# Kernel tuning notes

Hardware: AMD Instinct MI355X
Metric: run time of the kernel (lower is better)

## Reference

```python
import jax, jax.numpy as jnp
import numpy as np

B, S, H, E, K = 4, 4096, 1024, 8, 2


def setup_inputs() -> dict:
    key = jax.random.key(0)
    ks = jax.random.split(key, 5)
    scale = 1.0 / np.sqrt(H)
    return {
        "x": jax.random.normal(ks[0], (B, S, H), dtype=jnp.float32),
        "gate_w": jax.random.normal(ks[1], (H, E), dtype=jnp.float32) * scale,
        "gate_b": jnp.zeros((E,), dtype=jnp.float32),
        "expert_w": jax.random.normal(ks[2], (E, H, H), dtype=jnp.float32) * scale,
        "expert_b": jnp.zeros((E, H), dtype=jnp.float32),
    }


def reference(x, gate_w, gate_b, expert_w, expert_b):
    bsz, seq_len, hsz = x.shape
    h = x.reshape(-1, hsz)                              # [T, H], T = B*S

    # --- router ---
    router_logits = h @ gate_w + gate_b                 # [T, E]
    probs = jax.nn.softmax(router_logits, axis=-1)
    top_w, top_idx = jax.lax.top_k(probs, K)            # [T, K]
    top_w = top_w / jnp.sum(top_w, axis=-1, keepdims=True)

    # combine weight per (token, expert): sum over top-k slots of w * onehot(idx)
    one_hot = jax.nn.one_hot(top_idx, E, dtype=h.dtype)  # [T, K, E]
    combine = jnp.einsum("tk,tke->te", top_w, one_hot)   # [T, E]

    # --- experts (dense grouped GEMM, masked-combined; same math as gather/scatter loop) ---
    expert_out = jnp.einsum("th,ehd->etd", h, expert_w) + expert_b[:, None, :]  # [E, T, H]
    out = jnp.einsum("te,etd->td", combine, expert_out)                          # [T, H]

    return out.reshape(bsz, seq_len, hsz), router_logits
```

## Files before the change

### kernel.cpp

```cpp
#include <hip/hip_runtime.h>

#define TT 16384
#define HH 1024
#define EE 8

typedef __attribute__((ext_vector_type(8))) short short8;
typedef __attribute__((ext_vector_type(4))) float f32x4;

__device__ inline unsigned short f2bf(float f) {
    union { float f; unsigned int u; } v; v.f = f;
    unsigned int u = v.u;
    unsigned int r = (u + 0x7FFFu + ((u >> 16) & 1u)) >> 16;
    return (unsigned short)r;
}

__global__ __launch_bounds__(256) void transpose_w_kernel(
    const float* __restrict__ w, unsigned short* __restrict__ wt)
{
    __shared__ unsigned short tile[64][66];
    int bid = blockIdx.x;
    int e   = bid >> 8;
    int rem = bid & 255;
    int hb  = ((rem >> 4) & 15) * 64;
    int db  = (rem & 15) * 64;
    int tid = threadIdx.x;
    int c4  = (tid & 15) * 4;
    int r0  = tid >> 4;

    const float* we = w + (size_t)e * HH * HH;
    #pragma unroll
    for (int i = 0; i < 4; ++i) {
        int r = i * 16 + r0;
        float4 v = *(const float4*)(we + (size_t)(hb + r) * HH + db + c4);
        tile[r][c4 + 0] = f2bf(v.x);
        tile[r][c4 + 1] = f2bf(v.y);
        tile[r][c4 + 2] = f2bf(v.z);
        tile[r][c4 + 3] = f2bf(v.w);
    }
    __syncthreads();
    unsigned short* wte = wt + (size_t)e * HH * HH;
    #pragma unroll
    for (int i = 0; i < 4; ++i) {
        int dr = i * 16 + r0;
        ushort4 o;
        o.x = tile[c4 + 0][dr];
        o.y = tile[c4 + 1][dr];
        o.z = tile[c4 + 2][dr];
        o.w = tile[c4 + 3][dr];
        *(ushort4*)(wte + (size_t)(db + dr) * HH + hb + c4) = o;
    }
}

__global__ __launch_bounds__(256) void router_decide_kernel(
    const float* __restrict__ x, const float* __restrict__ gw,
    const float* __restrict__ gb, const float* __restrict__ eb,
    float* __restrict__ out, float* __restrict__ logits,
    unsigned short* __restrict__ xb, int* __restrict__ tops_i,
    float* __restrict__ tops_w)
{
    const int lane = threadIdx.x & 63;
    const int wv   = threadIdx.x >> 6;
    const int t    = blockIdx.x * 4 + wv;

    const float* xrow = x + (size_t)t * HH;
    unsigned short* xbrow = xb + (size_t)t * HH;

    float acc[8];
    #pragma unroll
    for (int e = 0; e < 8; ++e) acc[e] = 0.0f;

    #pragma unroll
    for (int i = 0; i < 4; ++i) {
        int idx = i * 256 + lane * 4;
        float4 v = *(const float4*)(xrow + idx);
        ushort4 bv;
        bv.x = f2bf(v.x); bv.y = f2bf(v.y); bv.z = f2bf(v.z); bv.w = f2bf(v.w);
        *(ushort4*)(xbrow + idx) = bv;
        float xs[4] = {v.x, v.y, v.z, v.w};
        #pragma unroll
        for (int j = 0; j < 4; ++j) {
            const float* g = gw + (size_t)(idx + j) * EE;
            float4 g0 = *(const float4*)(g);
            float4 g1 = *(const float4*)(g + 4);
            acc[0] += xs[j] * g0.x; acc[1] += xs[j] * g0.y;
            acc[2] += xs[j] * g0.z; acc[3] += xs[j] * g0.w;
            acc[4] += xs[j] * g1.x; acc[5] += xs[j] * g1.y;
            acc[6] += xs[j] * g1.z; acc[7] += xs[j] * g1.w;
        }
    }
    #pragma unroll
    for (int e = 0; e < 8; ++e) {
        #pragma unroll
        for (int off = 32; off >= 1; off >>= 1)
            acc[e] += __shfl_xor(acc[e], off, 64);
    }
    float lg[8];
    #pragma unroll
    for (int e = 0; e < 8; ++e) lg[e] = acc[e] + gb[e];

    float myv = 0.0f;
    #pragma unroll
    for (int e = 0; e < 8; ++e) myv = (lane == e) ? lg[e] : myv;
    if (lane < 8) logits[(size_t)t * EE + lane] = myv;

    int i0 = 0;
    #pragma unroll
    for (int e = 1; e < 8; ++e) if (lg[e] > lg[i0]) i0 = e;
    int i1 = (i0 == 0) ? 1 : 0;
    #pragma unroll
    for (int e = 0; e < 8; ++e) if (e != i0 && lg[e] > lg[i1]) i1 = e;

    float w0 = 1.0f / (1.0f + expf(lg[i1] - lg[i0]));
    float w1 = 1.0f - w0;

    if (lane == 0) {
        tops_i[t] = i0 | (i1 << 3);
        tops_w[t] = w0;
    }

    const float* b0 = eb + (size_t)i0 * HH;
    const float* b1 = eb + (size_t)i1 * HH;
    float* orow = out + (size_t)t * HH;
    #pragma unroll
    for (int i = 0; i < 4; ++i) {
        int idx = i * 256 + lane * 4;
        float4 a = *(const float4*)(b0 + idx);
        float4 c = *(const float4*)(b1 + idx);
        float4 r;
        r.x = w0 * a.x + w1 * c.x;
        r.y = w0 * a.y + w1 * c.y;
        r.z = w0 * a.z + w1 * c.z;
        r.w = w0 * a.w + w1 * c.w;
        *(float4*)(orow + idx) = r;
    }
}

__global__ __launch_bounds__(256) void build_lists_kernel(
    const int* __restrict__ tops_i, const float* __restrict__ tops_w,
    int* __restrict__ counts, int* __restrict__ tokl, float* __restrict__ wl)
{
    __shared__ int lcnt[EE];
    __shared__ int gbase[EE];
    int tid = threadIdx.x;
    if (tid < EE) lcnt[tid] = 0;
    __syncthreads();

    int t   = blockIdx.x * 256 + tid;
    int rec = tops_i[t];
    int i0  = rec & 7;
    int i1  = (rec >> 3) & 7;
    float w0 = tops_w[t];
    float w1 = 1.0f - w0;

    int r0 = atomicAdd(&lcnt[i0], 1);
    int r1 = atomicAdd(&lcnt[i1], 1);
    __syncthreads();

    if (tid < EE) gbase[tid] = atomicAdd(&counts[tid], lcnt[tid]);
    __syncthreads();

    int p0 = gbase[i0] + r0;
    tokl[i0 * TT + p0] = t; wl[i0 * TT + p0] = w0;
    int p1 = gbase[i1] + r1;
    tokl[i1 * TT + p1] = t; wl[i1 * TT + p1] = w1;
}

#define BM 128
#define BN 128
#define BK 64

__global__ __launch_bounds__(256) void moe_gemm_kernel(
    const unsigned short* __restrict__ xb, const unsigned short* __restrict__ wt,
    const int* __restrict__ counts, const int* __restrict__ tokl,
    const float* __restrict__ wl, float* __restrict__ out)
{
    const int NB    = HH / BN;
    const int MAXMB = TT / BM;
    int bid = blockIdx.x;
    int e   = bid / (MAXMB * NB);
    int rem = bid - e * (MAXMB * NB);
    int mb  = rem / NB;
    int nb  = rem - mb * NB;
    int cnt = counts[e];
    int row0 = mb * BM;
    if (row0 >= cnt) return;

    __shared__ __align__(16) unsigned short Alds[BM * BK];
    __shared__ __align__(16) unsigned short Blds[BN * BK];
    __shared__ int   toks[BM];
    __shared__ float wgts[BM];

    int tid = threadIdx.x;
    if (tid < BM) {
        int g = row0 + tid;
        bool ok = g < cnt;
        toks[tid] = ok ? tokl[e * TT + g] : 0;
        wgts[tid] = ok ? wl[e * TT + g] : 0.0f;
    }
    __syncthreads();

    const int lane = tid & 63;
    const int wv   = tid >> 6;
    const int wr   = wv >> 1, wc = wv & 1;
    const int mrow = wr * 64, ncol = wc * 64;

    f32x4 acc[4][4];
    #pragma unroll
    for (int m = 0; m < 4; ++m)
        #pragma unroll
        for (int n = 0; n < 4; ++n) acc[m][n] = (f32x4)0.0f;

    const unsigned short* wte = wt + (size_t)e * HH * HH + (size_t)(nb * BN) * HH;
    const int off = wv * 1024 + lane * 16;

    for (int kt = 0; kt < HH / BK; ++kt) {
        int k0 = kt * BK;
        #pragma unroll
        for (int rnd = 0; rnd < 4; ++rnd) {
            int o  = rnd * 4096 + off;
            int r  = o >> 7;
            int cb = o & 127;
            const unsigned short* srcA = xb + (size_t)toks[r] * HH + k0 + (cb >> 1);
            __builtin_amdgcn_global_load_lds(
                (const __attribute__((address_space(1))) void*)srcA,
                (__attribute__((address_space(3))) void*)((char*)Alds + rnd * 4096 + wv * 1024),
                16, 0, 0);
            const unsigned short* srcB = wte + (size_t)r * HH + k0 + (cb >> 1);
            __builtin_amdgcn_global_load_lds(
                (const __attribute__((address_space(1))) void*)srcB,
                (__attribute__((address_space(3))) void*)((char*)Blds + rnd * 4096 + wv * 1024),
                16, 0, 0);
        }
        __syncthreads();
        #pragma unroll
        for (int kk = 0; kk < 2; ++kk) {
            int kb = kk * 64 + (lane >> 4) * 16;
            short8 av[4], bv[4];
            #pragma unroll
            for (int m = 0; m < 4; ++m)
                av[m] = *(const short8*)((const char*)Alds + (mrow + m * 16 + (lane & 15)) * 128 + kb);
            #pragma unroll
            for (int n = 0; n < 4; ++n)
                bv[n] = *(const short8*)((const char*)Blds + (ncol + n * 16 + (lane & 15)) * 128 + kb);
            #pragma unroll
            for (int m = 0; m < 4; ++m)
                #pragma unroll
                for (int n = 0; n < 4; ++n)
                    acc[m][n] = __builtin_amdgcn_mfma_f32_16x16x32_bf16(av[m], bv[n], acc[m][n], 0, 0, 0);
        }
        __syncthreads();
    }

    #pragma unroll
    for (int m = 0; m < 4; ++m) {
        int lr0 = mrow + m * 16 + ((lane >> 4) << 2);
        #pragma unroll
        for (int rg = 0; rg < 4; ++rg) {
            int lr = lr0 + rg;
            int tkn = toks[lr];
            float wg = wgts[lr];
            if (wg != 0.0f) {
                float* orow = out + (size_t)tkn * HH + nb * BN + ncol + (lane & 15);
                #pragma unroll
                for (int n = 0; n < 4; ++n)
                    atomicAdd(orow + n * 16, wg * acc[m][n][rg]);
            }
        }
    }
}

extern "C" void kernel_launch(void* const* d_in, const int* in_sizes, int n_in,
                              void* d_out, int out_size, void* d_ws, size_t ws_size,
                              hipStream_t stream) {
    const float* x  = (const float*)d_in[0];
    const float* gw = (const float*)d_in[1];
    const float* gb = (const float*)d_in[2];
    const float* ew = (const float*)d_in[3];
    const float* eb = (const float*)d_in[4];
    float* out    = (float*)d_out;
    float* logits = out + (size_t)TT * HH;

    char* w = (char*)d_ws;
    unsigned short* xb = (unsigned short*)w;
    unsigned short* wt = (unsigned short*)(w + (size_t)TT * HH * 2);
    char* p  = w + (size_t)TT * HH * 2 + (size_t)EE * HH * HH * 2;
    int*   counts = (int*)p;
    int*   tokl   = (int*)(p + 256);
    float* wl     = (float*)(p + 256 + (size_t)EE * TT * 4);
    int*   tops_i = (int*)(p + 256 + 2 * (size_t)EE * TT * 4);
    float* tops_w = (float*)(p + 256 + 2 * (size_t)EE * TT * 4 + TT * 4);

    hipMemsetAsync(counts, 0, 256, stream);
    hipLaunchKernelGGL(transpose_w_kernel, dim3(EE * 256), dim3(256), 0, stream, ew, wt);
    hipLaunchKernelGGL(router_decide_kernel, dim3(TT / 4), dim3(256), 0, stream,
                       x, gw, gb, eb, out, logits, xb, tops_i, tops_w);
    hipLaunchKernelGGL(build_lists_kernel, dim3(TT / 256), dim3(256), 0, stream,
                       tops_i, tops_w, counts, tokl, wl);
    hipLaunchKernelGGL(moe_gemm_kernel, dim3(EE * (TT / BM) * (HH / BN)), dim3(256), 0, stream,
                       xb, wt, counts, tokl, wl, out);
}
```

Measured before the change: 381.6 us.

## Stage gate weights in LDS per router block and interleave expert GEMM block order

The router kernel now loads the gate weight matrix once per block into shared memory, transposed to [E][H], and each wave handles four tokens, so the per-token global gate-weight loads become contiguous LDS float4 reads. The MoE GEMM block index is remapped so experts are interleaved across consecutive block IDs. Early-exit empty blocks are then spread evenly instead of clustered, which is meant to balance work across CUs. The costs are a 32KB LDS footprint per router block and a per-block preload of the gate weights.

```diff
diff --git a/kernel.cpp b/kernel.cpp
--- a/kernel.cpp
+++ b/kernel.cpp
@@ -58,80 +58,88 @@
     unsigned short* __restrict__ xb, int* __restrict__ tops_i,
     float* __restrict__ tops_w)
 {
-    const int lane = threadIdx.x & 63;
-    const int wv   = threadIdx.x >> 6;
-    const int t    = blockIdx.x * 4 + wv;
-
-    const float* xrow = x + (size_t)t * HH;
-    unsigned short* xbrow = xb + (size_t)t * HH;
-
-    float acc[8];
-    #pragma unroll
-    for (int e = 0; e < 8; ++e) acc[e] = 0.0f;
-
-    #pragma unroll
-    for (int i = 0; i < 4; ++i) {
-        int idx = i * 256 + lane * 4;
-        float4 v = *(const float4*)(xrow + idx);
-        ushort4 bv;
-        bv.x = f2bf(v.x); bv.y = f2bf(v.y); bv.z = f2bf(v.z); bv.w = f2bf(v.w);
-        *(ushort4*)(xbrow + idx) = bv;
-        float xs[4] = {v.x, v.y, v.z, v.w};
-        #pragma unroll
-        for (int j = 0; j < 4; ++j) {
-            const float* g = gw + (size_t)(idx + j) * EE;
-            float4 g0 = *(const float4*)(g);
-            float4 g1 = *(const float4*)(g + 4);
-            acc[0] += xs[j] * g0.x; acc[1] += xs[j] * g0.y;
-            acc[2] += xs[j] * g0.z; acc[3] += xs[j] * g0.w;
-            acc[4] += xs[j] * g1.x; acc[5] += xs[j] * g1.y;
-            acc[6] += xs[j] * g1.z; acc[7] += xs[j] * g1.w;
-        }
-    }
-    #pragma unroll
-    for (int e = 0; e < 8; ++e) {
-        #pragma unroll
-        for (int off = 32; off >= 1; off >>= 1)
-            acc[e] += __shfl_xor(acc[e], off, 64);
-    }
-    float lg[8];
-    #pragma unroll
-    for (int e = 0; e < 8; ++e) lg[e] = acc[e] + gb[e];
-
-    float myv = 0.0f;
-    #pragma unroll
-    for (int e = 0; e < 8; ++e) myv = (lane == e) ? lg[e] : myv;
-    if (lane < 8) logits[(size_t)t * EE + lane] = myv;
-
-    int i0 = 0;
-    #pragma unroll
-    for (int e = 1; e < 8; ++e) if (lg[e] > lg[i0]) i0 = e;
-    int i1 = (i0 == 0) ? 1 : 0;
-    #pragma unroll
-    for (int e = 0; e < 8; ++e) if (e != i0 && lg[e] > lg[i1]) i1 = e;
-
-    float w0 = 1.0f / (1.0f + expf(lg[i1] - lg[i0]));
-    float w1 = 1.0f - w0;
-
-    if (lane == 0) {
-        tops_i[t] = i0 | (i1 << 3);
-        tops_w[t] = w0;
-    }
-
-    const float* b0 = eb + (size_t)i0 * HH;
-    const float* b1 = eb + (size_t)i1 * HH;
-    float* orow = out + (size_t)t * HH;
-    #pragma unroll
-    for (int i = 0; i < 4; ++i) {
-        int idx = i * 256 + lane * 4;
-        float4 a = *(const float4*)(b0 + idx);
-        float4 c = *(const float4*)(b1 + idx);
-        float4 r;
-        r.x = w0 * a.x + w1 * c.x;
-        r.y = w0 * a.y + w1 * c.y;
-        r.z = w0 * a.z + w1 * c.z;
-        r.w = w0 * a.w + w1 * c.w;
-        *(float4*)(orow + idx) = r;
+    __shared__ float gwt[EE][HH];
+    int tid = threadIdx.x;
+    for (int i = tid; i < (HH * EE) / 4; i += 256) {
+        float4 v = ((const float4*)gw)[i];
+        int b4 = i * 4;
+        gwt[(b4 + 0) & 7][(b4 + 0) >> 3] = v.x;
+        gwt[(b4 + 1) & 7][(b4 + 1) >> 3] = v.y;
+        gwt[(b4 + 2) & 7][(b4 + 2) >> 3] = v.z;
+        gwt[(b4 + 3) & 7][(b4 + 3) >> 3] = v.w;
+    }
+    __syncthreads();
+
+    const int lane = tid & 63;
+    const int wv   = tid >> 6;
+
+    for (int tk = 0; tk < 4; ++tk) {
+        const int t = blockIdx.x * 16 + wv * 4 + tk;
+        const float* xrow = x + (size_t)t * HH;
+        unsigned short* xbrow = xb + (size_t)t * HH;
+
+        float acc[8];
+        #pragma unroll
+        for (int e = 0; e < 8; ++e) acc[e] = 0.0f;
+
+        #pragma unroll
+        for (int i = 0; i < 4; ++i) {
+            int idx = i * 256 + lane * 4;
+            float4 v = *(const float4*)(xrow + idx);
+            ushort4 bv;
+            bv.x = f2bf(v.x); bv.y = f2bf(v.y); bv.z = f2bf(v.z); bv.w = f2bf(v.w);
+            *(ushort4*)(xbrow + idx) = bv;
+            #pragma unroll
+            for (int e = 0; e < 8; ++e) {
+                float4 g = *(const float4*)(&gwt[e][idx]);
+                acc[e] += v.x * g.x + v.y * g.y + v.z * g.z + v.w * g.w;
+            }
+        }
+        #pragma unroll
+        for (int e = 0; e < 8; ++e) {
+            #pragma unroll
+            for (int off = 32; off >= 1; off >>= 1)
+                acc[e] += __shfl_xor(acc[e], off, 64);
+        }
+        float lg[8];
+        #pragma unroll
+        for (int e = 0; e < 8; ++e) lg[e] = acc[e] + gb[e];
+
+        float myv = 0.0f;
+        #pragma unroll
+        for (int e = 0; e < 8; ++e) myv = (lane == e) ? lg[e] : myv;
+        if (lane < 8) logits[(size_t)t * EE + lane] = myv;
+
+        int i0 = 0;
+        #pragma unroll
+        for (int e = 1; e < 8; ++e) if (lg[e] > lg[i0]) i0 = e;
+        int i1 = (i0 == 0) ? 1 : 0;
+        #pragma unroll
+        for (int e = 0; e < 8; ++e) if (e != i0 && lg[e] > lg[i1]) i1 = e;
+
+        float w0 = 1.0f / (1.0f + expf(lg[i1] - lg[i0]));
+        float w1 = 1.0f - w0;
+
+        if (lane == 0) {
+            tops_i[t] = i0 | (i1 << 3);
+            tops_w[t] = w0;
+        }
+
+        const float* b0 = eb + (size_t)i0 * HH;
+        const float* b1 = eb + (size_t)i1 * HH;
+        float* orow = out + (size_t)t * HH;
+        #pragma unroll
+        for (int i = 0; i < 4; ++i) {
+            int idx = i * 256 + lane * 4;
+            float4 a = *(const float4*)(b0 + idx);
+            float4 c = *(const float4*)(b1 + idx);
+            float4 r;
+            r.x = w0 * a.x + w1 * c.x;
+            r.y = w0 * a.y + w1 * c.y;
+            r.z = w0 * a.z + w1 * c.z;
+            r.w = w0 * a.w + w1 * c.w;
+            *(float4*)(orow + idx) = r;
+        }
     }
 }
 
@@ -174,13 +182,11 @@
     const int* __restrict__ counts, const int* __restrict__ tokl,
     const float* __restrict__ wl, float* __restrict__ out)
 {
-    const int NB    = HH / BN;
-    const int MAXMB = TT / BM;
     int bid = blockIdx.x;
-    int e   = bid / (MAXMB * NB);
-    int rem = bid - e * (MAXMB * NB);
-    int mb  = rem / NB;
-    int nb  = rem - mb * NB;
+    int e   = bid & 7;
+    int j   = bid >> 3;
+    int mb  = j >> 3;
+    int nb  = j & 7;
     int cnt = counts[e];
     int row0 = mb * BM;
     if (row0 >= cnt) return;
@@ -292,7 +298,7 @@
 
     hipMemsetAsync(counts, 0, 256, stream);
     hipLaunchKernelGGL(transpose_w_kernel, dim3(EE * 256), dim3(256), 0, stream, ew, wt);
-    hipLaunchKernelGGL(router_decide_kernel, dim3(TT / 4), dim3(256), 0, stream,
+    hipLaunchKernelGGL(router_decide_kernel, dim3(TT / 16), dim3(256), 0, stream,
                        x, gw, gb, eb, out, logits, xb, tops_i, tops_w);
     hipLaunchKernelGGL(build_lists_kernel, dim3(TT / 256), dim3(256), 0, stream,
                        tops_i, tops_w, counts, tokl, wl);
```

Measured after the change: 323.1 us. 1.18x faster.
